# Kernel tuning notes

Hardware: AMD Instinct MI355X
Metric: run time of the kernel (lower is better)

Reference implementation:

```python
import jax, jax.numpy as jnp
import numpy as np

EPS = 1e-12  # matches torch F.normalize eps

def _l2norm(x, axis):
    n = jnp.sqrt(jnp.sum(x * x, axis=axis, keepdims=True))
    return x / jnp.maximum(n, EPS)

def setup_inputs() -> dict:
    key = jax.random.key(0)
    b, N, c, h, w = 8, 4, 256, 64, 64
    n, hw, L = N - 1, h * w, 2048
    k1, k2, k3, k4, k5 = jax.random.split(key, 5)
    feat = jax.random.normal(k1, (b, c, h, w), dtype=jnp.float32)
    refs = jax.random.normal(k2, (b, N, c, h, w), dtype=jnp.float32)
    similarity = jax.random.uniform(k3, (b, N), dtype=jnp.float32)
    # unique indices per row (the torch code pads by repeating mask indices; we use
    # unique ones so the final scatter is deterministic)
    base_indices = jax.vmap(lambda k: jax.random.permutation(k, hw))(jax.random.split(k4, b))[:, :L].astype(jnp.int64)
    ref_idx = jax.vmap(lambda k: jax.random.permutation(k, hw))(jax.random.split(k5, b * n))
    ref_indices_in = ref_idx.reshape(b, n, hw)[:, :, :L].astype(jnp.int64)
    return {"feat": feat, "refs": refs, "similarity": similarity,
            "base_indices": base_indices, "ref_indices_in": ref_indices_in, "index": 0}

def reference(feat, refs, similarity, base_indices, ref_indices_in, index):
    b, N, c, h, w = refs.shape
    n, hw = N - 1, h * w
    L = base_indices.shape[1]
    # drop the base reference slot
    refs_r = jnp.concatenate([refs[:, :index], refs[:, index + 1:]], axis=1)      # [b,n,c,h,w]
    base_sim = similarity[:, index]                                              # [b]
    ref_sims = jnp.concatenate([similarity[:, :index], similarity[:, index + 1:]], axis=1)  # [b,n]

    feat_flat = feat.reshape(b, c, hw)                                           # [b,c,hw]
    w_feat = _l2norm(feat_flat.transpose(0, 2, 1), axis=2)                       # [b,hw,c]
    w_refs = _l2norm(refs_r.reshape(b, n, c, hw), axis=2)                        # [b,n,c,hw]

    # gather masked positions
    feat_select = jnp.take_along_axis(feat_flat, base_indices[:, None, :], axis=2)      # [b,c,L]
    w_feat_sel = _l2norm(jnp.take_along_axis(w_feat, base_indices[:, :, None], axis=1), axis=2)  # [b,L,c]
    w_ref_sel = jnp.take_along_axis(w_refs, ref_indices_in[:, :, None, :], axis=3)      # [b,n,c,L]

    # cosine similarity + top-1 match per base position, per reference
    fx = jnp.einsum('blc,bncm->bnlm', w_feat_sel, w_ref_sel)                     # [b,n,L,L]
    ref_indices = jnp.argmax(fx, axis=3)                                         # [b,n,L] (top-1)
    ref_selects = jnp.take_along_axis(w_ref_sel, ref_indices[:, :, None, :], axis=3)    # [b,n,c,L]

    # similarity-weighted fusion
    feat_fused = base_sim[:, None, None] * feat_select \
               + jnp.einsum('bn,bncl->bcl', ref_sims, ref_selects)               # [b,c,L]

    # scatter fused features back into the base feature map
    bi = jnp.arange(b)[:, None, None]
    ci = jnp.arange(c)[None, :, None]
    out = feat_flat.at[bi, ci, base_indices[:, None, :]].set(feat_fused)
    return out.reshape(b, c, h, w), base_indices, ref_indices
```

## Files before the change

kernel.cpp:

```cpp
#include <hip/hip_runtime.h>
#include <math.h>

#define HWp 4096
#define Cp 256
#define Lp 2048
#define Np 3
#define Bp 8

#define OUT_FEAT_N 8388608
#define OUT_BASE_OFF 8388608
#define OUT_REF_OFF 8404992
#define NROWS 49152

#define OFF_AT    ((size_t)0)
#define OFF_BT    ((size_t)16777216)
#define OFF_BSPL  ((size_t)67108864)
#define OFF_PVAL  ((size_t)117440512)
#define OFF_BEST  ((size_t)119799808)
#define OFF_CAND2 ((size_t)119996416)
#define OFF_COUNT ((size_t)120193024)
#define OFF_LIST  ((size_t)120193280)
#define OFF_INV   ((size_t)120389888)

typedef _Float16 f16x8 __attribute__((ext_vector_type(8)));
typedef float f32x4 __attribute__((ext_vector_type(4)));

__device__ __forceinline__ unsigned short f16bits(float x){
    union { _Float16 h; unsigned short s; } u;
    u.h = (_Float16)x;
    return u.s;
}

__global__ void init_inv_kernel(int4* __restrict__ inv4){
    int tid = blockIdx.x * blockDim.x + threadIdx.x;
    if (tid < 32768) inv4[tid] = make_int4(-1, -1, -1, -1);
}

__global__ void scatter_inv_kernel(const int* __restrict__ refIdxI,
                                   const int* __restrict__ baseIdx,
                                   int* __restrict__ inv){
    int tid = blockIdx.x * blockDim.x + threadIdx.x;
    if (tid < NROWS){
        int g = tid >> 11;
        inv[g*4096 + refIdxI[tid]] = tid & 2047;
    } else if (tid < NROWS + Bp*Lp){
        int t = tid - NROWS;
        int b = t >> 11;
        inv[(24 + b)*4096 + baseIdx[t]] = t & 2047;
    }
}

__global__ __launch_bounds__(256) void gather_kernel(
    const float* __restrict__ feat, const float* __restrict__ refs,
    const int* __restrict__ pindex, const int* __restrict__ inv,
    float* __restrict__ A_T, float* __restrict__ B_T,
    unsigned char* __restrict__ Btiles)
{
    int tileh = blockIdx.x & 63;
    int g = blockIdx.x >> 6;
    int isRef = (g < 24);
    const float* src;
    int b;
    if (isRef){
        b = g / 3; int r0 = g - b*3; int iv = *pindex;
        int rn = (r0 < iv) ? r0 : r0 + 1;
        src = refs + ((size_t)(b*4 + rn)) * Cp * HWp;
    } else {
        b = g - 24;
        src = feat + (size_t)b * Cp * HWp;
    }
    __shared__ float lds[64 * 256];
    int tid = threadIdx.x, hwl = tid & 63, cg = tid >> 6;
    int hw0 = tileh * 64;
    const float* sp = src + hw0 + hwl;
    int swz = (hwl & 7) << 3;
    float* lrow = lds + hwl * 256;
    #pragma unroll
    for (int i = 0; i < 16; i++){
        int c0 = cg * 64 + i * 4;
        float x0 = sp[(size_t)(c0 + 0) * HWp];
        float x1 = sp[(size_t)(c0 + 1) * HWp];
        float x2 = sp[(size_t)(c0 + 2) * HWp];
        float x3 = sp[(size_t)(c0 + 3) * HWp];
        *(float4*)(lrow + (c0 ^ swz)) = make_float4(x0, x1, x2, x3);
    }
    __syncthreads();
    int w = cg, lane = tid & 63;
    const int* invg = inv + g * 4096 + hw0;
    for (int h = w * 16; h < w * 16 + 16; h++){
        int dest = invg[h];
        if (dest < 0) continue;
        float4 v = *(float4*)(lds + h * 256 + ((lane * 4) ^ ((h & 7) << 3)));
        float ssq = v.x*v.x + v.y*v.y + v.z*v.z + v.w*v.w;
        #pragma unroll
        for (int off = 1; off < 64; off <<= 1) ssq += __shfl_xor(ssq, off, 64);
        float dn = fmaxf(sqrtf(ssq), 1e-12f);
        v.x /= dn; v.y /= dn; v.z /= dn; v.w /= dn;
        if (isRef){
            size_t row = ((size_t)g * Lp + dest) * Cp;
            *(float4*)(B_T + row + lane * 4) = v;
            unsigned char* tb = Btiles + ((size_t)g * 64 + (dest >> 5)) * 16384;
            int nn = dest & 31;
            int ct2 = nn >> 4, c16 = nn & 15;
            int byteoff = (lane >> 3) * 2048 + ct2 * 1024
                        + (((lane >> 1) & 3) * 16 + c16) * 16 + (lane & 1) * 8;
            ushort4 hv;
            hv.x = f16bits(v.x); hv.y = f16bits(v.y);
            hv.z = f16bits(v.z); hv.w = f16bits(v.w);
            *(ushort4*)(tb + byteoff) = hv;
        } else {
            size_t row = ((size_t)b * Lp + dest) * Cp;
            *(float4*)(A_T + row + lane * 4) = v;
        }
    }
}

__device__ __forceinline__ void stageB(const unsigned char* g, unsigned char* l){
    #pragma unroll
    for (int p = 0; p < 4; p++)
        __builtin_amdgcn_global_load_lds(
            (const __attribute__((address_space(1))) void*)(g + p*1024),
            (__attribute__((address_space(3))) void*)(l + p*1024),
            16, 0, 0);
}

__global__ __launch_bounds__(256, 3) void gemm_mfma_kernel(
    const float* __restrict__ A_T, const unsigned char* __restrict__ Btiles,
    unsigned int* __restrict__ ppk)
{
    int orig = (blockIdx.x & 7) * 192 + (blockIdx.x >> 3);
    int rowgrp = orig & 15;
    int chunk = (orig >> 4) % 12;
    int b = orig / 192;
    int n = chunk >> 2, c4 = chunk & 3;
    int bn = b*3 + n;
    int tid = threadIdx.x, lane = tid & 63, w = tid >> 6;
    int l15 = lane & 15, lg = lane >> 4;

    __shared__ unsigned char bufs[2][16384];

    int row0 = rowgrp*128 + w*16 + l15;
    const float* Arow0 = A_T + ((size_t)b*Lp + row0)*Cp + lg*8;
    const float* Arow1 = Arow0 + (size_t)64*Cp;
    union U8 { _Float16 h[8]; f16x8 v; };
    U8 A0[8], A1[8];
    #pragma unroll
    for (int ks = 0; ks < 8; ks++){
        float4 fa = *(const float4*)(Arow0 + ks*32);
        float4 fb = *(const float4*)(Arow0 + ks*32 + 4);
        float xs[8] = {fa.x, fa.y, fa.z, fa.w, fb.x, fb.y, fb.z, fb.w};
        #pragma unroll
        for (int jj = 0; jj < 8; jj++) A0[ks].h[jj] = (_Float16)xs[jj];
        float4 fc = *(const float4*)(Arow1 + ks*32);
        float4 fd = *(const float4*)(Arow1 + ks*32 + 4);
        float ys[8] = {fc.x, fc.y, fc.z, fc.w, fd.x, fd.y, fd.z, fd.w};
        #pragma unroll
        for (int jj = 0; jj < 8; jj++) A1[ks].h[jj] = (_Float16)ys[jj];
    }

    unsigned p1[8], p2[8];
    #pragma unroll
    for (int s = 0; s < 8; s++){ p1[s] = 0u; p2[s] = 0u; }

    const unsigned char* tbase0 = Btiles + ((size_t)bn*64 + c4*16) * 16384;
    stageB(tbase0 + w*4096 + lane*16, &bufs[0][w*4096]);

    #pragma unroll 1
    for (int t = 0; t < 16; t++){
        if (t < 15){
            stageB(tbase0 + (size_t)(t+1)*16384 + w*4096 + lane*16, &bufs[(t+1)&1][w*4096]);
            asm volatile("s_waitcnt vmcnt(4)" ::: "memory");
        } else {
            asm volatile("s_waitcnt vmcnt(0)" ::: "memory");
        }
        __builtin_amdgcn_s_barrier();

        const unsigned char* bp = bufs[t & 1];
        f32x4 a00 = {2.f,2.f,2.f,2.f}, a01 = {2.f,2.f,2.f,2.f};
        f32x4 a10 = {2.f,2.f,2.f,2.f}, a11 = {2.f,2.f,2.f,2.f};
        #pragma unroll
        for (int ks = 0; ks < 8; ks++){
            f16x8 b0 = *(const f16x8*)(bp + ks*2048 + lane*16);
            f16x8 b1 = *(const f16x8*)(bp + ks*2048 + 1024 + lane*16);
            a00 = __builtin_amdgcn_mfma_f32_16x16x32_f16(A0[ks].v, b0, a00, 0, 0, 0);
            a01 = __builtin_amdgcn_mfma_f32_16x16x32_f16(A0[ks].v, b1, a01, 0, 0, 0);
            a10 = __builtin_amdgcn_mfma_f32_16x16x32_f16(A1[ks].v, b0, a10, 0, 0, 0);
            a11 = __builtin_amdgcn_mfma_f32_16x16x32_f16(A1[ks].v, b1, a11, 0, 0, 0);
        }
        __builtin_amdgcn_s_barrier();

        unsigned ci0 = (unsigned)(511 - (t*32 + l15));
        unsigned ci1 = ci0 - 16;
        #pragma unroll
        for (int r = 0; r < 4; r++){
            {
                unsigned u0 = (__float_as_uint(a00[r]) & 0xFFFFFE00u) | ci0;
                unsigned u1 = (__float_as_uint(a01[r]) & 0xFFFFFE00u) | ci1;
                unsigned hi = max(u0, u1), lo = min(u0, u1);
                unsigned tm = min(p1[r], hi);
                p1[r] = max(p1[r], hi);
                p2[r] = max(p2[r], max(lo, tm));
            }
            {
                unsigned u0 = (__float_as_uint(a10[r]) & 0xFFFFFE00u) | ci0;
                unsigned u1 = (__float_as_uint(a11[r]) & 0xFFFFFE00u) | ci1;
                unsigned hi = max(u0, u1), lo = min(u0, u1);
                unsigned tm = min(p1[4+r], hi);
                p1[4+r] = max(p1[4+r], hi);
                p2[4+r] = max(p2[4+r], max(lo, tm));
            }
        }
    }

    #pragma unroll
    for (int s = 0; s < 8; s++){
        unsigned q1 = p1[s], q2 = p2[s];
        #pragma unroll
        for (int off = 1; off < 16; off <<= 1){
            unsigned o1 = (unsigned)__shfl_xor((int)q1, off, 64);
            unsigned o2 = (unsigned)__shfl_xor((int)q2, off, 64);
            unsigned m1 = max(q1, o1);
            unsigned m2 = max(min(q1, o1), max(q2, o2));
            q1 = m1; q2 = m2;
        }
        if (l15 == 0){
            int rs = s >> 2, r = s & 3;
            size_t grow = (size_t)bn*Lp + rowgrp*128 + rs*64 + w*16 + lg*4 + r;
            size_t slot = grow*4 + c4;
            ppk[slot*2 + 0] = q1;
            ppk[slot*2 + 1] = q2;
        }
    }
}

__global__ void reset_kernel(int* count){ *count = 0; }

__global__ void combine_kernel(const unsigned int* __restrict__ ppk,
                               int* __restrict__ best, int* __restrict__ cand2,
                               float* __restrict__ outF, const int* __restrict__ baseIdx,
                               int* __restrict__ count, int* __restrict__ list)
{
    int gid = blockIdx.x * blockDim.x + threadIdx.x;
    if (gid < NROWS){
        unsigned V1 = 0u, V2 = 0u; int X1 = 0, X2 = 0;
        #pragma unroll
        for (int ch = 0; ch < 4; ch++){
            unsigned u1 = ppk[((size_t)gid*4 + ch)*2 + 0];
            unsigned u2 = ppk[((size_t)gid*4 + ch)*2 + 1];
            unsigned vb1 = u1 & 0xFFFFFE00u; int c1 = ch*512 + 511 - (int)(u1 & 511u);
            unsigned vb2 = u2 & 0xFFFFFE00u; int c2 = ch*512 + 511 - (int)(u2 & 511u);
            if (vb1 > V1 || (vb1 == V1 && c1 < X1)){
                V2 = V1; X2 = X1; V1 = vb1; X1 = c1;
            } else if (vb1 > V2 || (vb1 == V2 && c1 < X2)){
                V2 = vb1; X2 = c1;
            }
            if (vb2 > V2 || (vb2 == V2 && c2 < X2)){ V2 = vb2; X2 = c2; }
        }
        best[gid] = X1; cand2[gid] = X2;
        outF[OUT_REF_OFF + gid] = (float)X1;
        if (__uint_as_float(V1) - __uint_as_float(V2) < 3.6e-4f){
            int s = atomicAdd(count, 1);
            if (s < NROWS) list[s] = gid;
        }
    }
    if (gid < Bp*Lp) outF[OUT_BASE_OFF + gid] = (float)baseIdx[gid];
}

__global__ void refine_kernel(const float* __restrict__ A_T, const float* __restrict__ B_T,
                              const int* __restrict__ count, const int* __restrict__ list,
                              int* __restrict__ best, const int* __restrict__ cand2,
                              float* __restrict__ outF)
{
    int nf = *count; if (nf > NROWS) nf = NROWS;
    int lane = threadIdx.x & 63;
    for (int it = blockIdx.x; it < nf; it += gridDim.x){
        int gid = list[it];
        int bn = gid >> 11, l = gid & 2047;
        int b = bn / 3;
        int i1 = best[gid], i2 = cand2[gid];
        const float* ar  = A_T + ((size_t)b*Lp + l) * Cp;
        const float* b1r = B_T + ((size_t)bn*Lp + i1) * Cp;
        const float* b2r = B_T + ((size_t)bn*Lp + i2) * Cp;
        double d1 = 0.0, d2 = 0.0;
        #pragma unroll
        for (int j = 0; j < 4; j++){
            double a = (double)ar[lane*4 + j];
            d1 += a * (double)b1r[lane*4 + j];
            d2 += a * (double)b2r[lane*4 + j];
        }
        #pragma unroll
        for (int off = 1; off < 64; off <<= 1){
            d1 += __shfl_xor(d1, off, 64);
            d2 += __shfl_xor(d2, off, 64);
        }
        if (lane == 0){
            int ix = (d2 > d1 || (d2 == d1 && i2 < i1)) ? i2 : i1;
            best[gid] = ix;
            outF[OUT_REF_OFF + gid] = (float)ix;
        }
    }
}

__global__ __launch_bounds__(256) void fuse_tile_kernel(
    const float* __restrict__ feat, const float* __restrict__ B_T,
    const int* __restrict__ best, const int* __restrict__ inv,
    const float* __restrict__ sim, const int* __restrict__ pindex,
    float* __restrict__ out)
{
    int tileh = blockIdx.x & 63;
    int b = blockIdx.x >> 6;
    int hw0 = tileh * 64;
    __shared__ float lds[256 * 64];
    int tid = threadIdx.x, hwl = tid & 63, cg = tid >> 6;
    const float* fb = feat + (size_t)b * Cp * HWp + hw0 + hwl;
    #pragma unroll 4
    for (int i = 0; i < 64; i++){
        int c = cg * 64 + i;
        lds[c * 64 + ((hwl + c) & 63)] = fb[(size_t)c * HWp];
    }
    __syncthreads();
    int iv = *pindex;
    float bs  = sim[b*4 + iv];
    float rs0 = sim[b*4 + ((0 < iv) ? 0 : 1)];
    float rs1 = sim[b*4 + ((1 < iv) ? 1 : 2)];
    float rs2 = sim[b*4 + ((2 < iv) ? 2 : 3)];
    int w = cg, lane = tid & 63;
    const int* invg = inv + (24 + b) * 4096 + hw0;
    for (int h = w * 16; h < w * 16 + 16; h++){
        int dest = invg[h];
        if (dest < 0) continue;
        int b0 = best[(b*3 + 0)*Lp + dest];
        int b1 = best[(b*3 + 1)*Lp + dest];
        int b2 = best[(b*3 + 2)*Lp + dest];
        const float* r0 = B_T + ((size_t)(b*3 + 0)*Lp + b0) * Cp;
        const float* r1 = B_T + ((size_t)(b*3 + 1)*Lp + b1) * Cp;
        const float* r2 = B_T + ((size_t)(b*3 + 2)*Lp + b2) * Cp;
        #pragma unroll
        for (int j = 0; j < 4; j++){
            int c = lane + j * 64;
            int la = c * 64 + ((h + c) & 63);
            float base = lds[la];
            lds[la] = bs*base + rs0*r0[c] + rs1*r1[c] + rs2*r2[c];
        }
    }
    __syncthreads();
    float* ob = out + (size_t)b * Cp * HWp + hw0 + hwl;
    #pragma unroll 4
    for (int i = 0; i < 64; i++){
        int c = cg * 64 + i;
        ob[(size_t)c * HWp] = lds[c * 64 + ((hwl + c) & 63)];
    }
}

extern "C" void kernel_launch(void* const* d_in, const int* in_sizes, int n_in,
                              void* d_out, int out_size, void* d_ws, size_t ws_size,
                              hipStream_t stream)
{
    const float* feat    = (const float*)d_in[0];
    const float* refs    = (const float*)d_in[1];
    const float* sim     = (const float*)d_in[2];
    const int*   baseIdx = (const int*)d_in[3];
    const int*   refIdxI = (const int*)d_in[4];
    const int*   pindex  = (const int*)d_in[5];
    float* out = (float*)d_out;
    unsigned char* ws = (unsigned char*)d_ws;

    float* A_T   = (float*)(ws + OFF_AT);
    float* B_T   = (float*)(ws + OFF_BT);
    unsigned char* Btiles = ws + OFF_BSPL;
    unsigned int* ppk = (unsigned int*)(ws + OFF_PVAL);
    int* best  = (int*)(ws + OFF_BEST);
    int* cand2 = (int*)(ws + OFF_CAND2);
    int* count = (int*)(ws + OFF_COUNT);
    int* list  = (int*)(ws + OFF_LIST);
    int* inv   = (int*)(ws + OFF_INV);

    init_inv_kernel<<<128, 256, 0, stream>>>((int4*)inv);
    scatter_inv_kernel<<<256, 256, 0, stream>>>(refIdxI, baseIdx, inv);
    gather_kernel<<<2048, 256, 0, stream>>>(feat, refs, pindex, inv, A_T, B_T, Btiles);
    gemm_mfma_kernel<<<1536, 256, 0, stream>>>(A_T, Btiles, ppk);
    reset_kernel<<<1, 1, 0, stream>>>(count);
    combine_kernel<<<192, 256, 0, stream>>>(ppk, best, cand2, out, baseIdx, count, list);
    refine_kernel<<<512, 64, 0, stream>>>(A_T, B_T, count, list, best, cand2, out);
    fuse_tile_kernel<<<512, 256, 0, stream>>>(feat, B_T, best, inv, sim, pindex, out);
}
```

Before: 170.8 us.

## Store fp16 B rows linearly and halve gather tile size

The gather kernel now writes the fp16 copy of normalized reference rows in a plain row-major layout instead of the pre-swizzled MFMA tile layout. The GEMM's async global-to-LDS staging computes per-lane addresses into that linear layout. Gather tiles shrink from 64 to 32 spatial positions, doubling the grid and cutting LDS per block, which should raise occupancy. The aim is more coalesced fp16 stores in gather and higher gather parallelism, at the cost of less contiguous 16-byte loads in the GEMM staging.

Measured after the change: 167.3 us. -2.1%, faster.

```diff
diff --git a/kernel.cpp b/kernel.cpp
--- a/kernel.cpp
+++ b/kernel.cpp
@@ -14,7 +14,7 @@
 
 #define OFF_AT    ((size_t)0)
 #define OFF_BT    ((size_t)16777216)
-#define OFF_BSPL  ((size_t)67108864)
+#define OFF_BF16  ((size_t)67108864)
 #define OFF_PVAL  ((size_t)117440512)
 #define OFF_BEST  ((size_t)119799808)
 #define OFF_CAND2 ((size_t)119996416)
@@ -54,10 +54,10 @@
     const float* __restrict__ feat, const float* __restrict__ refs,
     const int* __restrict__ pindex, const int* __restrict__ inv,
     float* __restrict__ A_T, float* __restrict__ B_T,
-    unsigned char* __restrict__ Btiles)
-{
-    int tileh = blockIdx.x & 63;
-    int g = blockIdx.x >> 6;
+    unsigned char* __restrict__ Bf16)
+{
+    int tileh = blockIdx.x & 127;
+    int g = blockIdx.x >> 7;
     int isRef = (g < 24);
     const float* src;
     int b;
@@ -69,15 +69,15 @@
         b = g - 24;
         src = feat + (size_t)b * Cp * HWp;
     }
-    __shared__ float lds[64 * 256];
-    int tid = threadIdx.x, hwl = tid & 63, cg = tid >> 6;
-    int hw0 = tileh * 64;
+    __shared__ float lds[32 * 256];
+    int tid = threadIdx.x, hwl = tid & 31, cg = tid >> 5;
+    int hw0 = tileh * 32;
     const float* sp = src + hw0 + hwl;
     int swz = (hwl & 7) << 3;
     float* lrow = lds + hwl * 256;
     #pragma unroll
-    for (int i = 0; i < 16; i++){
-        int c0 = cg * 64 + i * 4;
+    for (int i = 0; i < 8; i++){
+        int c0 = cg * 32 + i * 4;
         float x0 = sp[(size_t)(c0 + 0) * HWp];
         float x1 = sp[(size_t)(c0 + 1) * HWp];
         float x2 = sp[(size_t)(c0 + 2) * HWp];
@@ -85,9 +85,9 @@
         *(float4*)(lrow + (c0 ^ swz)) = make_float4(x0, x1, x2, x3);
     }
     __syncthreads();
-    int w = cg, lane = tid & 63;
+    int w = tid >> 6, lane = tid & 63;
     const int* invg = inv + g * 4096 + hw0;
-    for (int h = w * 16; h < w * 16 + 16; h++){
+    for (int h = w * 8; h < w * 8 + 8; h++){
         int dest = invg[h];
         if (dest < 0) continue;
         float4 v = *(float4*)(lds + h * 256 + ((lane * 4) ^ ((h & 7) << 3)));
@@ -99,15 +99,10 @@
         if (isRef){
             size_t row = ((size_t)g * Lp + dest) * Cp;
             *(float4*)(B_T + row + lane * 4) = v;
-            unsigned char* tb = Btiles + ((size_t)g * 64 + (dest >> 5)) * 16384;
-            int nn = dest & 31;
-            int ct2 = nn >> 4, c16 = nn & 15;
-            int byteoff = (lane >> 3) * 2048 + ct2 * 1024
-                        + (((lane >> 1) & 3) * 16 + c16) * 16 + (lane & 1) * 8;
             ushort4 hv;
             hv.x = f16bits(v.x); hv.y = f16bits(v.y);
             hv.z = f16bits(v.z); hv.w = f16bits(v.w);
-            *(ushort4*)(tb + byteoff) = hv;
+            *(ushort4*)(Bf16 + ((size_t)g * Lp + dest) * 512 + lane * 8) = hv;
         } else {
             size_t row = ((size_t)b * Lp + dest) * Cp;
             *(float4*)(A_T + row + lane * 4) = v;
@@ -115,17 +110,17 @@
     }
 }
 
-__device__ __forceinline__ void stageB(const unsigned char* g, unsigned char* l){
+__device__ __forceinline__ void stage4(const unsigned char* srcLane, unsigned char* ldsW){
     #pragma unroll
     for (int p = 0; p < 4; p++)
         __builtin_amdgcn_global_load_lds(
-            (const __attribute__((address_space(1))) void*)(g + p*1024),
-            (__attribute__((address_space(3))) void*)(l + p*1024),
+            (const __attribute__((address_space(1))) void*)(srcLane + (p & 1) * 8192 + (p >> 1) * 64),
+            (__attribute__((address_space(3))) void*)(ldsW + p * 1024),
             16, 0, 0);
 }
 
 __global__ __launch_bounds__(256, 3) void gemm_mfma_kernel(
-    const float* __restrict__ A_T, const unsigned char* __restrict__ Btiles,
+    const float* __restrict__ A_T, const unsigned char* __restrict__ Bf16,
     unsigned int* __restrict__ ppk)
 {
     int orig = (blockIdx.x & 7) * 192 + (blockIdx.x >> 3);
@@ -162,13 +157,18 @@
     #pragma unroll
     for (int s = 0; s < 8; s++){ p1[s] = 0u; p2[s] = 0u; }
 
-    const unsigned char* tbase0 = Btiles + ((size_t)bn*64 + c4*16) * 16384;
-    stageB(tbase0 + w*4096 + lane*16, &bufs[0][w*4096]);
+    const unsigned char* srcLane = Bf16
+        + ((size_t)(bn*2048 + c4*512)) * 512
+        + l15 * 512 + (lane >> 4) * 16 + w * 128;
+    unsigned char* ldsW0 = &bufs[0][w*4096];
+    unsigned char* ldsW1 = &bufs[1][w*4096];
+
+    stage4(srcLane, ldsW0);
 
     #pragma unroll 1
     for (int t = 0; t < 16; t++){
         if (t < 15){
-            stageB(tbase0 + (size_t)(t+1)*16384 + w*4096 + lane*16, &bufs[(t+1)&1][w*4096]);
+            stage4(srcLane + (size_t)(t+1)*16384, (t & 1) ? ldsW0 : ldsW1);
             asm volatile("s_waitcnt vmcnt(4)" ::: "memory");
         } else {
             asm volatile("s_waitcnt vmcnt(0)" ::: "memory");
@@ -367,7 +367,7 @@
 
     float* A_T   = (float*)(ws + OFF_AT);
     float* B_T   = (float*)(ws + OFF_BT);
-    unsigned char* Btiles = ws + OFF_BSPL;
+    unsigned char* Bf16 = ws + OFF_BF16;
     unsigned int* ppk = (unsigned int*)(ws + OFF_PVAL);
     int* best  = (int*)(ws + OFF_BEST);
     int* cand2 = (int*)(ws + OFF_CAND2);
@@ -377,8 +377,8 @@
 
     init_inv_kernel<<<128, 256, 0, stream>>>((int4*)inv);
     scatter_inv_kernel<<<256, 256, 0, stream>>>(refIdxI, baseIdx, inv);
-    gather_kernel<<<2048, 256, 0, stream>>>(feat, refs, pindex, inv, A_T, B_T, Btiles);
-    gemm_mfma_kernel<<<1536, 256, 0, stream>>>(A_T, Btiles, ppk);
+    gather_kernel<<<4096, 256, 0, stream>>>(feat, refs, pindex, inv, A_T, B_T, Bf16);
+    gemm_mfma_kernel<<<1536, 256, 0, stream>>>(A_T, Bf16, ppk);
     reset_kernel<<<1, 1, 0, stream>>>(count);
     combine_kernel<<<192, 256, 0, stream>>>(ppk, best, cand2, out, baseIdx, count, list);
     refine_kernel<<<512, 64, 0, stream>>>(A_T, B_T, count, list, best, cand2, out);
```
